# Performance work log

Measured on AMD Instinct MI355X. Metric: run time of the kernel, lower is better.

## Reference

```python
import jax, jax.numpy as jnp
import numpy as np

N_NODES = 50000
N_EDGES = 1600000
IN_DIM = 16
HID = 128
N_ITER = 3
EPS = 1e-8


def _rownorm(x):
    # x / (||x||_2 per row + 1e-8), matching torch.norm(p='fro', dim=1, keepdim=True)
    return x / (jnp.linalg.norm(x, axis=-1, keepdims=True) + EPS)


def setup_inputs() -> dict:
    key = jax.random.key(0)
    ks = jax.random.split(key, 16)
    s = 0.05  # small init scale for numerical sanity
    inp = {
        'feat': jax.random.normal(ks[0], (N_NODES, IN_DIM), dtype=jnp.float32),
        'src': jax.random.randint(ks[1], (N_EDGES,), 0, N_NODES, dtype=jnp.int32),
        'dst': jax.random.randint(ks[2], (N_EDGES,), 0, N_NODES, dtype=jnp.int32),
        'init_W0': jax.random.normal(ks[3], (IN_DIM, HID), dtype=jnp.float32) * s,
        'init_b0': jnp.zeros((HID,), dtype=jnp.float32),
        'init_W1': jax.random.normal(ks[4], (HID, HID), dtype=jnp.float32) * s,
        'init_b1': jnp.zeros((HID,), dtype=jnp.float32),
        'init_W2': jax.random.normal(ks[5], (HID, HID), dtype=jnp.float32) * s,
        'init_b2': jnp.zeros((HID,), dtype=jnp.float32),
        'node_W0': jax.random.normal(ks[6], (N_ITER, 3 * HID, HID), dtype=jnp.float32) * s,
        'node_b0': jnp.zeros((N_ITER, HID), dtype=jnp.float32),
        'node_W1': jax.random.normal(ks[7], (N_ITER, HID, HID), dtype=jnp.float32) * s,
        'node_b1': jnp.zeros((N_ITER, HID), dtype=jnp.float32),
        'node_W2': jax.random.normal(ks[8], (N_ITER, HID, HID), dtype=jnp.float32) * s,
        'node_b2': jnp.zeros((N_ITER, HID), dtype=jnp.float32),
    }
    return inp


def reference(feat, src, dst,
              init_W0, init_b0, init_W1, init_b1, init_W2, init_b2,
              node_W0, node_b0, node_W1, node_b1, node_W2, node_b2):
    n = feat.shape[0]

    # init_network: MLP (Linear+ReLU for hidden layers, linear output)
    h = jax.nn.relu(feat @ init_W0 + init_b0)
    h = jax.nn.relu(h @ init_W1 + init_b1)
    h = h @ init_W2 + init_b2  # [N, HID]

    # global representation: normalized sum over all nodes (single graph)
    gr = _rownorm(jnp.sum(h, axis=0, keepdims=True))  # [1, HID]

    # DGL update_all only updates nodes with >=1 incoming edge
    deg = jax.ops.segment_sum(jnp.ones_like(src, dtype=jnp.float32), dst,
                              num_segments=n)
    has_in = (deg > 0)[:, None]  # [N, 1]

    for i in range(node_W0.shape[0]):
        # copy_u + mailbox sum == gather src features, segment-sum by dst
        msg = jax.ops.segment_sum(h[src], dst, num_segments=n)  # [N, HID]
        inp = jnp.concatenate(
            [msg, h, jnp.broadcast_to(gr, (n, gr.shape[1]))], axis=1)  # [N, 3*HID]
        out = jax.nn.relu(inp @ node_W0[i] + node_b0[i])
        out = jax.nn.relu(out @ node_W1[i] + node_b1[i])
        out = out @ node_W2[i] + node_b2[i]
        out = _rownorm(out)
        h = jnp.where(has_in, out, h)
        gr = _rownorm(jnp.sum(h, axis=0, keepdims=True))

    return h
```

## Files before the change

kernel.cpp:

```cpp
#include <hip/hip_runtime.h>
#include <hip/hip_bf16.h>

#define HID 128
#define IN_DIM 16
#define LDST 136
#define NBSH 6
#define BPAD 16
#define SRCM 0x3ffffffu
#define CH 8192
#define NBMAX 1024
#define NDPW 4

typedef unsigned short u16;
typedef __attribute__((ext_vector_type(8))) short short8;
typedef __attribute__((ext_vector_type(4))) float f32x4;

__device__ __forceinline__ u16 f2b(float f) {
    unsigned u = __float_as_uint(f);
    return (u16)((u + 0x7FFF + ((u >> 16) & 1)) >> 16);
}


__global__ __launch_bounds__(256) void hist_k(const int* __restrict__ dst, int* __restrict__ bktcnt,
                                              int E, int nb) {
    __shared__ int hist[NBMAX];
    int tid = threadIdx.x;
    int base = blockIdx.x * CH;
    int cnt = E - base; if (cnt > CH) cnt = CH;
    for (int i = tid; i < nb; i += 256) hist[i] = 0;
    __syncthreads();
    for (int j = tid; j < cnt; j += 256) atomicAdd(&hist[dst[base + j] >> NBSH], 1);
    __syncthreads();
    for (int i = tid; i < nb; i += 256) {
        int c = hist[i];
        if (c > 0) atomicAdd(&bktcnt[i], c);
    }
}

__global__ __launch_bounds__(1024) void bscan_k(const int* __restrict__ bktcnt, int* __restrict__ bktbase,
                                                int* __restrict__ bcnt, int* __restrict__ row_ptr,
                                                int nb, int n, int E) {
    __shared__ int sbuf[1024];
    int t = threadIdx.x;
    int v = (t < nb) ? bktcnt[t] : 0;
    sbuf[t] = v;
    __syncthreads();
    for (int off = 1; off < 1024; off <<= 1) {
        int a = (t >= off) ? sbuf[t - off] : 0;
        __syncthreads();
        sbuf[t] += a;
        __syncthreads();
    }
    if (t < nb) {
        int excl = sbuf[t] - v;
        bktbase[t] = excl;
        bcnt[t * BPAD] = excl;
    }
    if (t == 0) { bktbase[nb] = E; row_ptr[n] = E; }
}

__global__ __launch_bounds__(256) void bin_k(const int* __restrict__ src, const int* __restrict__ dst,
                                             int* __restrict__ bcnt, unsigned* __restrict__ ebuf,
                                             int E, int nb) {
    __shared__ unsigned stage[CH];
    __shared__ u16 sbk[CH];
    __shared__ int hist[NBMAX];
    __shared__ int lofs[NBMAX];
    __shared__ int sbase[NBMAX];
    __shared__ int scan256[256];
    int tid = threadIdx.x;
    int base = blockIdx.x * CH;
    int cnt = E - base; if (cnt > CH) cnt = CH;

    for (int i = tid; i < nb; i += 256) hist[i] = 0;
    __syncthreads();
    for (int j = tid; j < cnt; j += 256) {
        int d = dst[base + j];
        atomicAdd(&hist[d >> NBSH], 1);
    }
    __syncthreads();
    int psum[4];
    int ts = 0;
#pragma unroll
    for (int q = 0; q < 4; q++) {
        int idx = tid * 4 + q;
        int hv = (idx < nb) ? hist[idx] : 0;
        psum[q] = ts;
        ts += hv;
    }
    scan256[tid] = ts;
    __syncthreads();
    for (int off = 1; off < 256; off <<= 1) {
        int a = (tid >= off) ? scan256[tid - off] : 0;
        __syncthreads();
        scan256[tid] += a;
        __syncthreads();
    }
    int tbase = (tid > 0) ? scan256[tid - 1] : 0;
#pragma unroll
    for (int q = 0; q < 4; q++) {
        int idx = tid * 4 + q;
        if (idx < nb) lofs[idx] = tbase + psum[q];
    }
    __syncthreads();
    for (int i = tid; i < nb; i += 256) {
        int c = hist[i];
        if (c > 0) {
            int g = atomicAdd(&bcnt[i * BPAD], c);
            sbase[i] = g - lofs[i];
        }
    }
    __syncthreads();
    for (int j = tid; j < cnt; j += 256) {
        int e = base + j;
        int d = dst[e];
        int b = d >> NBSH;
        int r = atomicAdd(&lofs[b], 1);
        stage[r] = (unsigned)src[e] | ((unsigned)(d & 63) << 26);
        sbk[r] = (u16)b;
    }
    __syncthreads();
    for (int s = tid; s < cnt; s += 256) {
        int b = sbk[s];
        ebuf[sbase[b] + s] = stage[s];
    }
}

__global__ __launch_bounds__(256) void fill2_k(const unsigned* __restrict__ ebuf, const int* __restrict__ bktbase,
                                               int* __restrict__ row_ptr, int* __restrict__ deg,
                                               int* __restrict__ srcs, int n) {
    __shared__ int hist64[64];
    __shared__ int lofs[64];
    int tid = threadIdx.x;
    int b = blockIdx.x;
    int e0 = bktbase[b], e1 = bktbase[b + 1];
    if (tid < 64) hist64[tid] = 0;
    __syncthreads();
    for (int i = e0 + tid; i < e1; i += 256) atomicAdd(&hist64[ebuf[i] >> 26], 1);
    __syncthreads();
    if (tid < 64) {
        int d = hist64[tid];
        int s = d;
#pragma unroll
        for (int off = 1; off < 64; off <<= 1) {
            int t = __shfl_up(s, off);
            if (tid >= off) s += t;
        }
        int excl = e0 + s - d;
        int gi = (b << NBSH) + tid;
        if (gi < n) { row_ptr[gi] = excl; deg[gi] = d; }
        lofs[tid] = excl;
    }
    __syncthreads();
    for (int i = e0 + tid; i < e1; i += 256) {
        unsigned p = ebuf[i];
        int d = (int)(p >> 26);
        int pos = atomicAdd(&lofs[d], 1);
        srcs[pos] = (int)(p & SRCM);
    }
}


struct WJobs {
    const float* src[16];
    int dstoff[16];
    int ks[16];
};

__global__ __launch_bounds__(256) void wprep_k(WJobs j, u16* __restrict__ Wt,
                                               int* __restrict__ bktcnt, float* __restrict__ gsums,
                                               int nb, int gz) {
    int m = blockIdx.x;
    if (m == 0) {
        for (int i = threadIdx.x; i < nb; i += 256) bktcnt[i] = 0;
    } else if (m == 1) {
        for (int i = threadIdx.x; i < gz; i += 256) gsums[i] = 0.f;
    }
    const float* s = j.src[m];
    u16* d = Wt + j.dstoff[m];
    int ks = j.ks[m];
    int K = 1 << ks;
    int tot = K * HID;
    for (int idx = threadIdx.x; idx < tot; idx += 256) {
        int nn = idx >> ks;
        int kk = idx & (K - 1);
        d[idx] = f2b(s[kk * HID + nn]);
    }
}


__device__ __forceinline__ void unpack_add(uint4 v, float* a) {
    a[0] += __uint_as_float(v.x << 16);
    a[1] += __uint_as_float(v.x & 0xffff0000u);
    a[2] += __uint_as_float(v.y << 16);
    a[3] += __uint_as_float(v.y & 0xffff0000u);
    a[4] += __uint_as_float(v.z << 16);
    a[5] += __uint_as_float(v.z & 0xffff0000u);
    a[6] += __uint_as_float(v.w << 16);
    a[7] += __uint_as_float(v.w & 0xffff0000u);
}

__global__ __launch_bounds__(256) void msg_k(const u16* __restrict__ hb, const int* __restrict__ row_ptr,
                                             const int* __restrict__ srcs, u16* __restrict__ msgb, int n,
                                             const float* __restrict__ gsumIn, const float* __restrict__ Wg,
                                             const float* __restrict__ b0, float* __restrict__ grW) {
    if (blockIdx.x == gridDim.x - 1) {
        __shared__ float sred[2];
        __shared__ float sgr[HID];
        int t = threadIdx.x;
        if (t < HID) {
            float g = gsumIn[t];
            float s = g * g;
#pragma unroll
            for (int off = 1; off < 64; off <<= 1) s += __shfl_xor(s, off);
            if ((t & 63) == 0) sred[t >> 6] = s;
        }
        __syncthreads();
        if (t < HID) {
            float inv = 1.f / (sqrtf(sred[0] + sred[1]) + 1e-8f);
            sgr[t] = gsumIn[t] * inv;
        }
        __syncthreads();
        if (t < HID) {
            float a = b0[t];
#pragma unroll 4
            for (int k = 0; k < HID; k++) a += sgr[k] * Wg[k * HID + t];
            grW[t] = a;
        }
        return;
    }
    int wave = threadIdx.x >> 6, lane = threadIdx.x & 63;
    int g = lane >> 4;
    int l16 = lane & 15;
    int d0 = (blockIdx.x * 4 + wave) * NDPW;
    if (d0 >= n) return;
    int eNext = row_ptr[d0];
#pragma unroll 1
    for (int k = 0; k < NDPW; k++) {
        int d = d0 + k;
        if (d >= n) break;
        int e = eNext;
        int e1 = row_ptr[d + 1];
        eNext = e1;
        float a[8] = {0.f, 0.f, 0.f, 0.f, 0.f, 0.f, 0.f, 0.f};
        int s0 = 0, s1 = 0, s2 = 0, s3 = 0;
        if (e + 15 < e1) {
            s0 = srcs[e + g]; s1 = srcs[e + 4 + g];
            s2 = srcs[e + 8 + g]; s3 = srcs[e + 12 + g];
        }
        while (e + 15 < e1) {
            int t0 = s0, t1 = s1, t2 = s2, t3 = s3;
            int en = e + 16;
            if (en + 15 < e1) {
                s0 = srcs[en + g]; s1 = srcs[en + 4 + g];
                s2 = srcs[en + 8 + g]; s3 = srcs[en + 12 + g];
            }
            uint4 v0 = *(const uint4*)(hb + (size_t)t0 * HID + l16 * 8);
            uint4 v1 = *(const uint4*)(hb + (size_t)t1 * HID + l16 * 8);
            uint4 v2 = *(const uint4*)(hb + (size_t)t2 * HID + l16 * 8);
            uint4 v3 = *(const uint4*)(hb + (size_t)t3 * HID + l16 * 8);
            unpack_add(v0, a);
            unpack_add(v1, a);
            unpack_add(v2, a);
            unpack_add(v3, a);
            e = en;
        }
        if (e + 7 < e1) {
            int t0 = srcs[e + g], t1 = srcs[e + 4 + g];
            uint4 v0 = *(const uint4*)(hb + (size_t)t0 * HID + l16 * 8);
            uint4 v1 = *(const uint4*)(hb + (size_t)t1 * HID + l16 * 8);
            unpack_add(v0, a);
            unpack_add(v1, a);
            e += 8;
        }
        if (e + 3 < e1) {
            int s = srcs[e + g];
            uint4 v = *(const uint4*)(hb + (size_t)s * HID + l16 * 8);
            unpack_add(v, a);
            e += 4;
        }
        if (e + g < e1) {
            int s = srcs[e + g];
            uint4 v = *(const uint4*)(hb + (size_t)s * HID + l16 * 8);
            unpack_add(v, a);
        }
#pragma unroll
        for (int i = 0; i < 8; i++) {
            a[i] += __shfl_xor(a[i], 16);
            a[i] += __shfl_xor(a[i], 32);
        }
        if (g == 0) {
            uint4 o;
            o.x = (unsigned)f2b(a[0]) | ((unsigned)f2b(a[1]) << 16);
            o.y = (unsigned)f2b(a[2]) | ((unsigned)f2b(a[3]) << 16);
            o.z = (unsigned)f2b(a[4]) | ((unsigned)f2b(a[5]) << 16);
            o.w = (unsigned)f2b(a[6]) | ((unsigned)f2b(a[7]) << 16);
            *(uint4*)(msgb + (size_t)d * HID + l16 * 8) = o;
        }
    }
}


__device__ __forceinline__ void load_tile(const u16* __restrict__ base, int tid, uint4 p[4]) {
#pragma unroll
    for (int q = 0; q < 4; q++) {
        int c = tid + q * 512;
        p[q] = *(const uint4*)(base + (size_t)(c >> 4) * HID + (c & 15) * 8);
    }
}

__device__ __forceinline__ void write_tile(const uint4 p[4], int tid, u16* s) {
#pragma unroll
    for (int q = 0; q < 4; q++) {
        int c = tid + q * 512;
        *(uint4*)(s + (c >> 4) * LDST + (c & 15) * 8) = p[q];
    }
}

__device__ __forceinline__ void stageFeat(const float* __restrict__ feat, int row0, int n, int tid, u16* sA) {
    int row = tid >> 2, coff = tid & 3;
    ushort4 o = make_ushort4(0, 0, 0, 0);
    if (row0 + row < n) {
        float4 v = *(const float4*)(feat + (size_t)(row0 + row) * IN_DIM + coff * 4);
        o = make_ushort4(f2b(v.x), f2b(v.y), f2b(v.z), f2b(v.w));
    }
    *(ushort4*)(sA + row * LDST + coff * 4) = o;
    *(ushort4*)(sA + row * LDST + 16 + coff * 4) = make_ushort4(0, 0, 0, 0);
}

__device__ __forceinline__ void stageW16(const u16* __restrict__ Wt, int tid, u16* sB) {
    if (tid < 256) {
        int row = tid >> 1, h8 = tid & 1;
        uint4 v = *(const uint4*)(Wt + row * IN_DIM + h8 * 8);
        *(uint4*)(sB + row * LDST + h8 * 8) = v;
        *(uint4*)(sB + row * LDST + 16 + h8 * 8) = make_uint4(0, 0, 0, 0);
    }
}

template <int KSTEPS>
__device__ __forceinline__ void mac(const u16* sA, const u16* sB, int wrow, int wcol,
                                    int ln15, int quad, f32x4 acc[2][4]) {
#pragma unroll
    for (int kk = 0; kk < KSTEPS; kk++) {
        short8 a[2], b[4];
#pragma unroll
        for (int mi = 0; mi < 2; mi++)
            a[mi] = *(const short8*)(sA + (wrow + mi * 16 + ln15) * LDST + kk * 32 + quad * 8);
#pragma unroll
        for (int ni = 0; ni < 4; ni++)
            b[ni] = *(const short8*)(sB + (wcol + ni * 16 + ln15) * LDST + kk * 32 + quad * 8);
#pragma unroll
        for (int mi = 0; mi < 2; mi++)
#pragma unroll
            for (int ni = 0; ni < 4; ni++)
                acc[mi][ni] = __builtin_amdgcn_mfma_f32_16x16x32_bf16(a[mi], b[ni], acc[mi][ni], 0, 0, 0);
    }
}

__device__ __forceinline__ void set_bias(f32x4 acc[2][4], const float* __restrict__ bias, int wcol, int ln15) {
#pragma unroll
    for (int ni = 0; ni < 4; ni++) {
        float bv = bias[wcol + ni * 16 + ln15];
#pragma unroll
        for (int mi = 0; mi < 2; mi++) acc[mi][ni] = (f32x4){bv, bv, bv, bv};
    }
}

__device__ __forceinline__ void acc_to_sA(const f32x4 acc[2][4], u16* sA, int wrow, int wcol,
                                          int ln15, int quad) {
#pragma unroll
    for (int mi = 0; mi < 2; mi++)
#pragma unroll
        for (int r = 0; r < 4; r++) {
            int row = wrow + mi * 16 + quad * 4 + r;
#pragma unroll
            for (int ni = 0; ni < 4; ni++)
                sA[row * LDST + wcol + ni * 16 + ln15] = f2b(fmaxf(acc[mi][ni][r], 0.f));
        }
}


__global__ __launch_bounds__(512, 4) void init_fused_k(const float* __restrict__ feat,
                                                       const u16* __restrict__ W0t, const u16* __restrict__ W1t,
                                                       const u16* __restrict__ W2t,
                                                       const float* __restrict__ b0, const float* __restrict__ b1,
                                                       const float* __restrict__ b2,
                                                       float* __restrict__ h, u16* __restrict__ hb,
                                                       float* __restrict__ gsum0, int n) {
    __shared__ u16 sA[128 * LDST];
    __shared__ u16 sB[128 * LDST];
    int tid = threadIdx.x;
    int lane = tid & 63, wave = tid >> 6;
    int ln15 = lane & 15, quad = lane >> 4;
    int wrow = (wave >> 1) * 32, wcol = (wave & 1) * 64;
    int row0 = blockIdx.x * 128;
    f32x4 acc[2][4];
    uint4 pB[4];

    stageFeat(feat, row0, n, tid, sA);
    stageW16(W0t, tid, sB);
    load_tile(W1t, tid, pB);
    set_bias(acc, b0, wcol, ln15);
    __syncthreads();
    mac<1>(sA, sB, wrow, wcol, ln15, quad, acc);
    __syncthreads();
    acc_to_sA(acc, sA, wrow, wcol, ln15, quad);
    write_tile(pB, tid, sB);
    load_tile(W2t, tid, pB);
    set_bias(acc, b1, wcol, ln15);
    __syncthreads();
    mac<4>(sA, sB, wrow, wcol, ln15, quad, acc);
    __syncthreads();
    acc_to_sA(acc, sA, wrow, wcol, ln15, quad);
    write_tile(pB, tid, sB);
    set_bias(acc, b2, wcol, ln15);
    __syncthreads();
    mac<4>(sA, sB, wrow, wcol, ln15, quad, acc);

    float csum[4] = {0.f, 0.f, 0.f, 0.f};
#pragma unroll
    for (int mi = 0; mi < 2; mi++)
#pragma unroll
        for (int r = 0; r < 4; r++) {
            int row = row0 + wrow + mi * 16 + quad * 4 + r;
            if (row < n) {
#pragma unroll
                for (int ni = 0; ni < 4; ni++) {
                    float v = acc[mi][ni][r];
                    int col = wcol + ni * 16 + ln15;
                    h[(size_t)row * HID + col] = v;
                    hb[(size_t)row * HID + col] = f2b(v);
                    csum[ni] += v;
                }
            }
        }
    __syncthreads();
    float* s_cs = (float*)sA;
    if (tid < HID) s_cs[tid] = 0.f;
    __syncthreads();
#pragma unroll
    for (int ni = 0; ni < 4; ni++) {
        float p = csum[ni];
        p += __shfl_xor(p, 16);
        p += __shfl_xor(p, 32);
        if (quad == 0) atomicAdd(&s_cs[wcol + ni * 16 + ln15], p);
    }
    __syncthreads();
    if (tid < HID) atomicAdd(&gsum0[tid], s_cs[tid]);
}


template <bool FINAL>
__global__ __launch_bounds__(512, 4) void node_fused_k(const u16* __restrict__ msgb, const u16* __restrict__ hbin,
                                                       const u16* __restrict__ W0a, const u16* __restrict__ W0b,
                                                       const u16* __restrict__ W1t, const u16* __restrict__ W2t,
                                                       const float* __restrict__ grW,
                                                       const float* __restrict__ b1, const float* __restrict__ b2,
                                                       const int* __restrict__ deg,
                                                       float* __restrict__ h, u16* __restrict__ hb,
                                                       float* __restrict__ gsumOut, int n) {
    __shared__ u16 sA[128 * LDST];
    __shared__ u16 sB[128 * LDST];
    int tid = threadIdx.x;
    int lane = tid & 63, wave = tid >> 6;
    int ln15 = lane & 15, quad = lane >> 4;
    int wrow = (wave >> 1) * 32, wcol = (wave & 1) * 64;
    int row0 = blockIdx.x * 128;
    f32x4 acc[2][4];
    uint4 pA[4], pB[4];

    load_tile(msgb + (size_t)row0 * HID, tid, pA);
    load_tile(W0a, tid, pB);
    write_tile(pA, tid, sA);
    write_tile(pB, tid, sB);
    load_tile(hbin + (size_t)row0 * HID, tid, pA);
    load_tile(W0b, tid, pB);
    set_bias(acc, grW, wcol, ln15);
    __syncthreads();
    mac<4>(sA, sB, wrow, wcol, ln15, quad, acc);
    __syncthreads();
    write_tile(pA, tid, sA);
    write_tile(pB, tid, sB);
    load_tile(W1t, tid, pB);
    __syncthreads();
    mac<4>(sA, sB, wrow, wcol, ln15, quad, acc);
    __syncthreads();
    acc_to_sA(acc, sA, wrow, wcol, ln15, quad);
    write_tile(pB, tid, sB);
    load_tile(W2t, tid, pB);
    set_bias(acc, b1, wcol, ln15);
    __syncthreads();
    mac<4>(sA, sB, wrow, wcol, ln15, quad, acc);
    __syncthreads();
    acc_to_sA(acc, sA, wrow, wcol, ln15, quad);
    write_tile(pB, tid, sB);
    set_bias(acc, b2, wcol, ln15);
    __syncthreads();
    mac<4>(sA, sB, wrow, wcol, ln15, quad, acc);

    __syncthreads();
    float* s_rs = (float*)sA;
    float* s_cs = (float*)sA + 128;
    if (tid < 128) s_rs[tid] = 0.f;
    else if (tid < 256) s_cs[tid - 128] = 0.f;
    __syncthreads();
#pragma unroll
    for (int mi = 0; mi < 2; mi++)
#pragma unroll
        for (int r = 0; r < 4; r++) {
            float p = 0.f;
#pragma unroll
            for (int ni = 0; ni < 4; ni++) { float v = acc[mi][ni][r]; p += v * v; }
            p += __shfl_xor(p, 1); p += __shfl_xor(p, 2);
            p += __shfl_xor(p, 4); p += __shfl_xor(p, 8);
            if (ln15 == 0) atomicAdd(&s_rs[wrow + mi * 16 + quad * 4 + r], p);
        }
    __syncthreads();
    float csum[4] = {0.f, 0.f, 0.f, 0.f};
#pragma unroll
    for (int mi = 0; mi < 2; mi++)
#pragma unroll
        for (int r = 0; r < 4; r++) {
            int rl = wrow + mi * 16 + quad * 4 + r;
            int row = row0 + rl;
            if (row < n) {
                bool upd = deg[row] > 0;
                float inv = 1.f / (sqrtf(s_rs[rl]) + 1e-8f);
#pragma unroll
                for (int ni = 0; ni < 4; ni++) {
                    int col = wcol + ni * 16 + ln15;
                    if (FINAL) {
                        if (upd) h[(size_t)row * HID + col] = acc[mi][ni][r] * inv;
                    } else {
                        float v;
                        if (upd) {
                            v = acc[mi][ni][r] * inv;
                            hb[(size_t)row * HID + col] = f2b(v);
                        } else {
                            v = h[(size_t)row * HID + col];
                        }
                        csum[ni] += v;
                    }
                }
            }
        }
    if (!FINAL) {
#pragma unroll
        for (int ni = 0; ni < 4; ni++) {
            float p = csum[ni];
            p += __shfl_xor(p, 16);
            p += __shfl_xor(p, 32);
            if (quad == 0) atomicAdd(&s_cs[wcol + ni * 16 + ln15], p);
        }
        __syncthreads();
        if (tid < HID) atomicAdd(&gsumOut[tid], s_cs[tid]);
    }
}


static inline char* align_up(char* p, size_t a) {
    return (char*)(((uintptr_t)p + a - 1) & ~(uintptr_t)(a - 1));
}

extern "C" void kernel_launch(void* const* d_in, const int* in_sizes, int n_in,
                              void* d_out, int out_size, void* d_ws, size_t ws_size,
                              hipStream_t stream) {
    const float* feat = (const float*)d_in[0];
    const int* src = (const int*)d_in[1];
    const int* dst = (const int*)d_in[2];
    const float* iW0 = (const float*)d_in[3];
    const float* ib0 = (const float*)d_in[4];
    const float* iW1 = (const float*)d_in[5];
    const float* ib1 = (const float*)d_in[6];
    const float* iW2 = (const float*)d_in[7];
    const float* ib2 = (const float*)d_in[8];
    const float* nW0 = (const float*)d_in[9];
    const float* nb0 = (const float*)d_in[10];
    const float* nW1 = (const float*)d_in[11];
    const float* nb1 = (const float*)d_in[12];
    const float* nW2 = (const float*)d_in[13];
    const float* nb2 = (const float*)d_in[14];

    int N = in_sizes[0] / IN_DIM;
    int E = in_sizes[1];
    int n_iter = in_sizes[10] / HID;
    int NB = (N + (1 << NBSH) - 1) >> NBSH;
    float* h = (float*)d_out;

    char* w = (char*)d_ws;
    size_t big2 = (size_t)(N + 128) * HID * sizeof(u16);
    u16* hb   = (u16*)w; w += big2;
    u16* msgb = (u16*)w; w += big2;
    float* gsums = (float*)w; w += (size_t)(n_iter + 1) * HID * sizeof(float);
    float* grW = (float*)w; w += 1024;
    u16* Wt = (u16*)w; w += (size_t)(2048 + 2 * 16384 + n_iter * 4 * 16384) * sizeof(u16);
    w = align_up(w, 16);
    int* deg = (int*)w; w += (size_t)N * 4;  w = align_up(w, 16);
    int* row_ptr = (int*)w; w += (size_t)(N + 1) * 4;  w = align_up(w, 16);
    int* bktcnt = (int*)w; w += (size_t)NB * 4;  w = align_up(w, 16);
    int* bktbase = (int*)w; w += (size_t)(NB + 1) * 4;  w = align_up(w, 64);
    int* bcnt = (int*)w; w += (size_t)NB * BPAD * 4;  w = align_up(w, 16);
    int* srcs = (int*)w; w += (size_t)E * 4;  w = align_up(w, 16);
    unsigned* ebuf = (unsigned*)w; w += (size_t)E * 4;
    (void)ws_size; (void)n_in; (void)out_size;

    const int OFF_IW0 = 0;
    const int OFF_IW1 = 2048;
    const int OFF_IW2 = 2048 + 16384;
    const int OFF_IT = 2048 + 2 * 16384;

    WJobs jobs;
    int nj = 0;
    jobs.src[nj] = iW0; jobs.dstoff[nj] = OFF_IW0; jobs.ks[nj] = 4; nj++;
    jobs.src[nj] = iW1; jobs.dstoff[nj] = OFF_IW1; jobs.ks[nj] = 7; nj++;
    jobs.src[nj] = iW2; jobs.dstoff[nj] = OFF_IW2; jobs.ks[nj] = 7; nj++;
    for (int i = 0; i < n_iter && nj + 4 <= 16; i++) {
        int base = OFF_IT + i * 4 * 16384;
        jobs.src[nj] = nW0 + (size_t)i * 3 * HID * HID;               jobs.dstoff[nj] = base;             jobs.ks[nj] = 7; nj++;
        jobs.src[nj] = nW0 + (size_t)i * 3 * HID * HID + HID * HID;   jobs.dstoff[nj] = base + 16384;     jobs.ks[nj] = 7; nj++;
        jobs.src[nj] = nW1 + (size_t)i * HID * HID;                   jobs.dstoff[nj] = base + 2 * 16384; jobs.ks[nj] = 7; nj++;
        jobs.src[nj] = nW2 + (size_t)i * HID * HID;                   jobs.dstoff[nj] = base + 3 * 16384; jobs.ks[nj] = 7; nj++;
    }

    wprep_k<<<nj, 256, 0, stream>>>(jobs, Wt, bktcnt, gsums, NB, (n_iter + 1) * HID);

    int cg = (E + CH - 1) / CH;
    hist_k<<<cg, 256, 0, stream>>>(dst, bktcnt, E, NB);
    bscan_k<<<1, 1024, 0, stream>>>(bktcnt, bktbase, bcnt, row_ptr, NB, N, E);
    bin_k<<<cg, 256, 0, stream>>>(src, dst, bcnt, ebuf, E, NB);
    fill2_k<<<NB, 256, 0, stream>>>(ebuf, bktbase, row_ptr, deg, srcs, N);

    int gb = (N + 127) / 128;
    int dpb = 4 * NDPW;
    int rb = (N + dpb - 1) / dpb;
    init_fused_k<<<gb, 512, 0, stream>>>(feat, Wt + OFF_IW0, Wt + OFF_IW1, Wt + OFF_IW2,
                                         ib0, ib1, ib2, h, hb, gsums, N);

    for (int i = 0; i < n_iter; i++) {
        const u16* Wit = Wt + OFF_IT + (size_t)i * 4 * 16384;
        const float* Wg = nW0 + (size_t)i * 3 * HID * HID + 2 * HID * HID;
        msg_k<<<rb + 1, 256, 0, stream>>>(hb, row_ptr, srcs, msgb, N,
                                          gsums + (size_t)i * HID, Wg, nb0 + (size_t)i * HID, grW);
        if (i + 1 < n_iter) {
            node_fused_k<false><<<gb, 512, 0, stream>>>(msgb, hb, Wit, Wit + 16384, Wit + 2 * 16384,
                                                        Wit + 3 * 16384, grW, nb1 + (size_t)i * HID,
                                                        nb2 + (size_t)i * HID, deg, h, hb,
                                                        gsums + (size_t)(i + 1) * HID, N);
        } else {
            node_fused_k<true><<<gb, 512, 0, stream>>>(msgb, hb, Wit, Wit + 16384, Wit + 2 * 16384,
                                                       Wit + 3 * 16384, grW, nb1 + (size_t)i * HID,
                                                       nb2 + (size_t)i * HID, deg, h, hb,
                                                       nullptr, N);
        }
    }
}
```

Before: 443.1 us.

## Fuse message aggregation and global-rep projection into node MLP kernel

Removes the separate msg_k launch. The neighbour gather-sum is now done inside the node MLP kernel, written straight into shared memory as the first MFMA operand, and each block recomputes the global-representation projection. The bf16 node features are double-buffered (ping-pong) so blocks can read the old features while writing the new ones. This avoids a global round trip for msgb and two kernel launches. In exchange, each 512-thread block with large LDS runs a serial, latency-bound gather over 128 rows, which may hide latency worse than the old fine-grained kernel. Every block also redundantly recomputes a 128x128 GEMV.

```diff
diff --git a/kernel.cpp b/kernel.cpp
--- a/kernel.cpp
+++ b/kernel.cpp
@@ -9,7 +9,6 @@
 #define SRCM 0x3ffffffu
 #define CH 8192
 #define NBMAX 1024
-#define NDPW 4
 
 typedef unsigned short u16;
 typedef __attribute__((ext_vector_type(8))) short short8;
@@ -188,7 +187,6 @@
     }
 }
 
-
 __device__ __forceinline__ void unpack_add(uint4 v, float* a) {
     a[0] += __uint_as_float(v.x << 16);
     a[1] += __uint_as_float(v.x & 0xffff0000u);
@@ -200,106 +198,6 @@
     a[7] += __uint_as_float(v.w & 0xffff0000u);
 }
 
-__global__ __launch_bounds__(256) void msg_k(const u16* __restrict__ hb, const int* __restrict__ row_ptr,
-                                             const int* __restrict__ srcs, u16* __restrict__ msgb, int n,
-                                             const float* __restrict__ gsumIn, const float* __restrict__ Wg,
-                                             const float* __restrict__ b0, float* __restrict__ grW) {
-    if (blockIdx.x == gridDim.x - 1) {
-        __shared__ float sred[2];
-        __shared__ float sgr[HID];
-        int t = threadIdx.x;
-        if (t < HID) {
-            float g = gsumIn[t];
-            float s = g * g;
-#pragma unroll
-            for (int off = 1; off < 64; off <<= 1) s += __shfl_xor(s, off);
-            if ((t & 63) == 0) sred[t >> 6] = s;
-        }
-        __syncthreads();
-        if (t < HID) {
-            float inv = 1.f / (sqrtf(sred[0] + sred[1]) + 1e-8f);
-            sgr[t] = gsumIn[t] * inv;
-        }
-        __syncthreads();
-        if (t < HID) {
-            float a = b0[t];
-#pragma unroll 4
-            for (int k = 0; k < HID; k++) a += sgr[k] * Wg[k * HID + t];
-            grW[t] = a;
-        }
-        return;
-    }
-    int wave = threadIdx.x >> 6, lane = threadIdx.x & 63;
-    int g = lane >> 4;
-    int l16 = lane & 15;
-    int d0 = (blockIdx.x * 4 + wave) * NDPW;
-    if (d0 >= n) return;
-    int eNext = row_ptr[d0];
-#pragma unroll 1
-    for (int k = 0; k < NDPW; k++) {
-        int d = d0 + k;
-        if (d >= n) break;
-        int e = eNext;
-        int e1 = row_ptr[d + 1];
-        eNext = e1;
-        float a[8] = {0.f, 0.f, 0.f, 0.f, 0.f, 0.f, 0.f, 0.f};
-        int s0 = 0, s1 = 0, s2 = 0, s3 = 0;
-        if (e + 15 < e1) {
-            s0 = srcs[e + g]; s1 = srcs[e + 4 + g];
-            s2 = srcs[e + 8 + g]; s3 = srcs[e + 12 + g];
-        }
-        while (e + 15 < e1) {
-            int t0 = s0, t1 = s1, t2 = s2, t3 = s3;
-            int en = e + 16;
-            if (en + 15 < e1) {
-                s0 = srcs[en + g]; s1 = srcs[en + 4 + g];
-                s2 = srcs[en + 8 + g]; s3 = srcs[en + 12 + g];
-            }
-            uint4 v0 = *(const uint4*)(hb + (size_t)t0 * HID + l16 * 8);
-            uint4 v1 = *(const uint4*)(hb + (size_t)t1 * HID + l16 * 8);
-            uint4 v2 = *(const uint4*)(hb + (size_t)t2 * HID + l16 * 8);
-            uint4 v3 = *(const uint4*)(hb + (size_t)t3 * HID + l16 * 8);
-            unpack_add(v0, a);
-            unpack_add(v1, a);
-            unpack_add(v2, a);
-            unpack_add(v3, a);
-            e = en;
-        }
-        if (e + 7 < e1) {
-            int t0 = srcs[e + g], t1 = srcs[e + 4 + g];
-            uint4 v0 = *(const uint4*)(hb + (size_t)t0 * HID + l16 * 8);
-            uint4 v1 = *(const uint4*)(hb + (size_t)t1 * HID + l16 * 8);
-            unpack_add(v0, a);
-            unpack_add(v1, a);
-            e += 8;
-        }
-        if (e + 3 < e1) {
-            int s = srcs[e + g];
-            uint4 v = *(const uint4*)(hb + (size_t)s * HID + l16 * 8);
-            unpack_add(v, a);
-            e += 4;
-        }
-        if (e + g < e1) {
-            int s = srcs[e + g];
-            uint4 v = *(const uint4*)(hb + (size_t)s * HID + l16 * 8);
-            unpack_add(v, a);
-        }
-#pragma unroll
-        for (int i = 0; i < 8; i++) {
-            a[i] += __shfl_xor(a[i], 16);
-            a[i] += __shfl_xor(a[i], 32);
-        }
-        if (g == 0) {
-            uint4 o;
-            o.x = (unsigned)f2b(a[0]) | ((unsigned)f2b(a[1]) << 16);
-            o.y = (unsigned)f2b(a[2]) | ((unsigned)f2b(a[3]) << 16);
-            o.z = (unsigned)f2b(a[4]) | ((unsigned)f2b(a[5]) << 16);
-            o.w = (unsigned)f2b(a[6]) | ((unsigned)f2b(a[7]) << 16);
-            *(uint4*)(msgb + (size_t)d * HID + l16 * 8) = o;
-        }
-    }
-}
-
 
 __device__ __forceinline__ void load_tile(const u16* __restrict__ base, int tid, uint4 p[4]) {
 #pragma unroll
@@ -357,7 +255,7 @@
     }
 }
 
-__device__ __forceinline__ void set_bias(f32x4 acc[2][4], const float* __restrict__ bias, int wcol, int ln15) {
+__device__ __forceinline__ void set_bias(f32x4 acc[2][4], const float* bias, int wcol, int ln15) {
 #pragma unroll
     for (int ni = 0; ni < 4; ni++) {
         float bv = bias[wcol + ni * 16 + ln15];
@@ -451,16 +349,19 @@
 
 
 template <bool FINAL>
-__global__ __launch_bounds__(512, 4) void node_fused_k(const u16* __restrict__ msgb, const u16* __restrict__ hbin,
-                                                       const u16* __restrict__ W0a, const u16* __restrict__ W0b,
-                                                       const u16* __restrict__ W1t, const u16* __restrict__ W2t,
-                                                       const float* __restrict__ grW,
-                                                       const float* __restrict__ b1, const float* __restrict__ b2,
-                                                       const int* __restrict__ deg,
-                                                       float* __restrict__ h, u16* __restrict__ hb,
-                                                       float* __restrict__ gsumOut, int n) {
+__global__ __launch_bounds__(512, 4) void node_merged_k(const u16* __restrict__ hbR, u16* __restrict__ hbW,
+                                                        const int* __restrict__ row_ptr, const int* __restrict__ srcs,
+                                                        const u16* __restrict__ W0a, const u16* __restrict__ W0b,
+                                                        const u16* __restrict__ W1t, const u16* __restrict__ W2t,
+                                                        const float* __restrict__ gsumIn, const float* __restrict__ Wg,
+                                                        const float* __restrict__ b0v, const float* __restrict__ b1,
+                                                        const float* __restrict__ b2, const int* __restrict__ deg,
+                                                        float* __restrict__ h, float* __restrict__ gsumOut, int n) {
     __shared__ u16 sA[128 * LDST];
     __shared__ u16 sB[128 * LDST];
+    __shared__ float sgp[4][HID];
+    __shared__ float sgrw[HID];
+    __shared__ float sred[2];
     int tid = threadIdx.x;
     int lane = tid & 63, wave = tid >> 6;
     int ln15 = lane & 15, quad = lane >> 4;
@@ -469,14 +370,111 @@
     f32x4 acc[2][4];
     uint4 pA[4], pB[4];
 
-    load_tile(msgb + (size_t)row0 * HID, tid, pA);
+    if (tid < HID) {
+        float g = gsumIn[tid];
+        float s = g * g;
+#pragma unroll
+        for (int off = 1; off < 64; off <<= 1) s += __shfl_xor(s, off);
+        if ((tid & 63) == 0) sred[tid >> 6] = s;
+    }
+    __syncthreads();
+    {
+        float inv = 1.f / (sqrtf(sred[0] + sred[1]) + 1e-8f);
+        int col = tid & 127, kq = tid >> 7;
+#pragma unroll 8
+        for (int k2 = 0; k2 < 32; k2++) {
+            if (k2 == 0) sgp[kq][col] = 0.f;
+        }
+        float p = 0.f;
+#pragma unroll 8
+        for (int k2 = 0; k2 < 32; k2++) {
+            int k = kq * 32 + k2;
+            p += gsumIn[k] * Wg[(size_t)k * HID + col];
+        }
+        sgp[kq][col] = p;
+        __syncthreads();
+        if (tid < HID) sgrw[tid] = b0v[tid] + inv * (sgp[0][tid] + sgp[1][tid] + sgp[2][tid] + sgp[3][tid]);
+    }
+
     load_tile(W0a, tid, pB);
-    write_tile(pA, tid, sA);
+    load_tile(hbR + (size_t)row0 * HID, tid, pA);
+
+    {
+        int gg = quad;
+        int gl = ln15;
+        int d0 = row0 + wave * 16;
+#pragma unroll 1
+        for (int k = 0; k < 16; k++) {
+            int d = d0 + k;
+            int rl = wave * 16 + k;
+            if (d >= n) {
+                if (gg == 0) *(uint4*)(sA + (size_t)rl * LDST + gl * 8) = make_uint4(0, 0, 0, 0);
+                continue;
+            }
+            int e = row_ptr[d];
+            int e1 = row_ptr[d + 1];
+            float a[8] = {0.f, 0.f, 0.f, 0.f, 0.f, 0.f, 0.f, 0.f};
+            int s0 = 0, s1 = 0, s2 = 0, s3 = 0;
+            if (e + 15 < e1) {
+                s0 = srcs[e + gg]; s1 = srcs[e + 4 + gg];
+                s2 = srcs[e + 8 + gg]; s3 = srcs[e + 12 + gg];
+            }
+            while (e + 15 < e1) {
+                int t0 = s0, t1 = s1, t2 = s2, t3 = s3;
+                int en = e + 16;
+                if (en + 15 < e1) {
+                    s0 = srcs[en + gg]; s1 = srcs[en + 4 + gg];
+                    s2 = srcs[en + 8 + gg]; s3 = srcs[en + 12 + gg];
+                }
+                uint4 v0 = *(const uint4*)(hbR + (size_t)t0 * HID + gl * 8);
+                uint4 v1 = *(const uint4*)(hbR + (size_t)t1 * HID + gl * 8);
+                uint4 v2 = *(const uint4*)(hbR + (size_t)t2 * HID + gl * 8);
+                uint4 v3 = *(const uint4*)(hbR + (size_t)t3 * HID + gl * 8);
+                unpack_add(v0, a);
+                unpack_add(v1, a);
+                unpack_add(v2, a);
+                unpack_add(v3, a);
+                e = en;
+            }
+            if (e + 7 < e1) {
+                int t0 = srcs[e + gg], t1 = srcs[e + 4 + gg];
+                uint4 v0 = *(const uint4*)(hbR + (size_t)t0 * HID + gl * 8);
+                uint4 v1 = *(const uint4*)(hbR + (size_t)t1 * HID + gl * 8);
+                unpack_add(v0, a);
+                unpack_add(v1, a);
+                e += 8;
+            }
+            if (e + 3 < e1) {
+                int s = srcs[e + gg];
+                uint4 v = *(const uint4*)(hbR + (size_t)s * HID + gl * 8);
+                unpack_add(v, a);
+                e += 4;
+            }
+            if (e + gg < e1) {
+                int s = srcs[e + gg];
+                uint4 v = *(const uint4*)(hbR + (size_t)s * HID + gl * 8);
+                unpack_add(v, a);
+            }
+#pragma unroll
+            for (int i = 0; i < 8; i++) {
+                a[i] += __shfl_xor(a[i], 16);
+                a[i] += __shfl_xor(a[i], 32);
+            }
+            if (gg == 0) {
+                uint4 o;
+                o.x = (unsigned)f2b(a[0]) | ((unsigned)f2b(a[1]) << 16);
+                o.y = (unsigned)f2b(a[2]) | ((unsigned)f2b(a[3]) << 16);
+                o.z = (unsigned)f2b(a[4]) | ((unsigned)f2b(a[5]) << 16);
+                o.w = (unsigned)f2b(a[6]) | ((unsigned)f2b(a[7]) << 16);
+                *(uint4*)(sA + (size_t)rl * LDST + gl * 8) = o;
+            }
+        }
+    }
+
     write_tile(pB, tid, sB);
-    load_tile(hbin + (size_t)row0 * HID, tid, pA);
     load_tile(W0b, tid, pB);
-    set_bias(acc, grW, wcol, ln15);
-    __syncthreads();
+    __syncthreads();
+    set_bias(acc, sgrw, wcol, ln15);
     mac<4>(sA, sB, wrow, wcol, ln15, quad, acc);
     __syncthreads();
     write_tile(pA, tid, sA);
@@ -535,10 +533,10 @@
                         float v;
                         if (upd) {
                             v = acc[mi][ni][r] * inv;
-                            hb[(size_t)row * HID + col] = f2b(v);
                         } else {
                             v = h[(size_t)row * HID + col];
                         }
+                        hbW[(size_t)row * HID + col] = f2b(v);
                         csum[ni] += v;
                     }
                 }
@@ -589,8 +587,8 @@
 
     char* w = (char*)d_ws;
     size_t big2 = (size_t)(N + 128) * HID * sizeof(u16);
-    u16* hb   = (u16*)w; w += big2;
-    u16* msgb = (u16*)w; w += big2;
+    u16* hb0  = (u16*)w; w += big2;
+    u16* hb1  = (u16*)w; w += big2;
     float* gsums = (float*)w; w += (size_t)(n_iter + 1) * HID * sizeof(float);
     float* grW = (float*)w; w += 1024;
     u16* Wt = (u16*)w; w += (size_t)(2048 + 2 * 16384 + n_iter * 4 * 16384) * sizeof(u16);
@@ -602,7 +600,7 @@
     int* bcnt = (int*)w; w += (size_t)NB * BPAD * 4;  w = align_up(w, 16);
     int* srcs = (int*)w; w += (size_t)E * 4;  w = align_up(w, 16);
     unsigned* ebuf = (unsigned*)w; w += (size_t)E * 4;
-    (void)ws_size; (void)n_in; (void)out_size;
+    (void)ws_size; (void)n_in; (void)out_size; (void)grW;
 
     const int OFF_IW0 = 0;
     const int OFF_IW1 = 2048;
@@ -631,26 +629,27 @@
     fill2_k<<<NB, 256, 0, stream>>>(ebuf, bktbase, row_ptr, deg, srcs, N);
 
     int gb = (N + 127) / 128;
-    int dpb = 4 * NDPW;
-    int rb = (N + dpb - 1) / dpb;
     init_fused_k<<<gb, 512, 0, stream>>>(feat, Wt + OFF_IW0, Wt + OFF_IW1, Wt + OFF_IW2,
-                                         ib0, ib1, ib2, h, hb, gsums, N);
-
+                                         ib0, ib1, ib2, h, hb0, gsums, N);
+
+    const u16* cur = hb0;
+    u16* nxt = hb1;
     for (int i = 0; i < n_iter; i++) {
         const u16* Wit = Wt + OFF_IT + (size_t)i * 4 * 16384;
         const float* Wg = nW0 + (size_t)i * 3 * HID * HID + 2 * HID * HID;
-        msg_k<<<rb + 1, 256, 0, stream>>>(hb, row_ptr, srcs, msgb, N,
-                                          gsums + (size_t)i * HID, Wg, nb0 + (size_t)i * HID, grW);
         if (i + 1 < n_iter) {
-            node_fused_k<false><<<gb, 512, 0, stream>>>(msgb, hb, Wit, Wit + 16384, Wit + 2 * 16384,
-                                                        Wit + 3 * 16384, grW, nb1 + (size_t)i * HID,
-                                                        nb2 + (size_t)i * HID, deg, h, hb,
-                                                        gsums + (size_t)(i + 1) * HID, N);
+            node_merged_k<false><<<gb, 512, 0, stream>>>(cur, nxt, row_ptr, srcs,
+                                                         Wit, Wit + 16384, Wit + 2 * 16384, Wit + 3 * 16384,
+                                                         gsums + (size_t)i * HID, Wg, nb0 + (size_t)i * HID,
+                                                         nb1 + (size_t)i * HID, nb2 + (size_t)i * HID, deg,
+                                                         h, gsums + (size_t)(i + 1) * HID, N);
         } else {
-            node_fused_k<true><<<gb, 512, 0, stream>>>(msgb, hb, Wit, Wit + 16384, Wit + 2 * 16384,
-                                                       Wit + 3 * 16384, grW, nb1 + (size_t)i * HID,
-                                                       nb2 + (size_t)i * HID, deg, h, hb,
-                                                       nullptr, N);
-        }
-    }
-}
+            node_merged_k<true><<<gb, 512, 0, stream>>>(cur, nxt, row_ptr, srcs,
+                                                        Wit, Wit + 16384, Wit + 2 * 16384, Wit + 3 * 16384,
+                                                        gsums + (size_t)i * HID, Wg, nb0 + (size_t)i * HID,
+                                                        nb1 + (size_t)i * HID, nb2 + (size_t)i * HID, deg,
+                                                        h, nullptr, N);
+        }
+        u16* t = (u16*)cur; cur = nxt; nxt = t;
+    }
+}
```

Measured after the change: 463.9 us. 1.05x slower.

## Pre-swizzle node MLP weights into MFMA fragment order and read from global

Applied to the files above, without the earlier changes.

Weight preparation for the per-iteration node MLP now writes the bf16 weights in the exact per-lane MFMA B-fragment order. The node kernel then loads B operands straight from global/L2 instead of staging them in shared memory. The node kernel also shrinks to 64-row tiles with 256 threads and a single shared buffer, cutting LDS use and the weight staging and barrier work per block. The cost is repeated global weight reads per block (L2-resident), plus twice as many blocks.

```diff
diff --git a/kernel.cpp b/kernel.cpp
--- a/kernel.cpp
+++ b/kernel.cpp
@@ -179,6 +179,19 @@
     const float* s = j.src[m];
     u16* d = Wt + j.dstoff[m];
     int ks = j.ks[m];
+    if (ks == 8) {
+        for (int idx = threadIdx.x; idx < 16384; idx += 256) {
+            int jj = idx & 7;
+            int lane = (idx >> 3) & 63;
+            int ni = (idx >> 9) & 3;
+            int kk = (idx >> 11) & 3;
+            int half = idx >> 13;
+            int k = kk * 32 + (lane >> 4) * 8 + jj;
+            int col = half * 64 + ni * 16 + (lane & 15);
+            d[idx] = f2b(s[k * HID + col]);
+        }
+        return;
+    }
     int K = 1 << ks;
     int tot = K * HID;
     for (int idx = threadIdx.x; idx < tot; idx += 256) {
@@ -317,6 +330,22 @@
     }
 }
 
+__device__ __forceinline__ void load_tile64(const u16* __restrict__ base, int tid, uint4 p[4]) {
+#pragma unroll
+    for (int q = 0; q < 4; q++) {
+        int c = tid + q * 256;
+        p[q] = *(const uint4*)(base + (size_t)(c >> 4) * HID + (c & 15) * 8);
+    }
+}
+
+__device__ __forceinline__ void write_tile64(const uint4 p[4], int tid, u16* s) {
+#pragma unroll
+    for (int q = 0; q < 4; q++) {
+        int c = tid + q * 256;
+        *(uint4*)(s + (c >> 4) * LDST + (c & 15) * 8) = p[q];
+    }
+}
+
 __device__ __forceinline__ void stageFeat(const float* __restrict__ feat, int row0, int n, int tid, u16* sA) {
     int row = tid >> 2, coff = tid & 3;
     ushort4 o = make_ushort4(0, 0, 0, 0);
@@ -357,7 +386,27 @@
     }
 }
 
-__device__ __forceinline__ void set_bias(f32x4 acc[2][4], const float* __restrict__ bias, int wcol, int ln15) {
+__device__ __forceinline__ void macF(const u16* sA, const u16* __restrict__ Wf, int wrow, int half,
+                                     int lane, int ln15, int quad, f32x4 acc[2][4]) {
+    const u16* wb = Wf + (size_t)half * 8192;
+#pragma unroll
+    for (int kk = 0; kk < 4; kk++) {
+        short8 a[2], b[4];
+#pragma unroll
+        for (int mi = 0; mi < 2; mi++)
+            a[mi] = *(const short8*)(sA + (wrow + mi * 16 + ln15) * LDST + kk * 32 + quad * 8);
+#pragma unroll
+        for (int ni = 0; ni < 4; ni++)
+            b[ni] = *(const short8*)(wb + (size_t)(((kk * 4 + ni) * 64) + lane) * 8);
+#pragma unroll
+        for (int mi = 0; mi < 2; mi++)
+#pragma unroll
+            for (int ni = 0; ni < 4; ni++)
+                acc[mi][ni] = __builtin_amdgcn_mfma_f32_16x16x32_bf16(a[mi], b[ni], acc[mi][ni], 0, 0, 0);
+    }
+}
+
+__device__ __forceinline__ void set_bias(f32x4 acc[2][4], const float* bias, int wcol, int ln15) {
 #pragma unroll
     for (int ni = 0; ni < 4; ni++) {
         float bv = bias[wcol + ni * 16 + ln15];
@@ -451,58 +500,52 @@
 
 
 template <bool FINAL>
-__global__ __launch_bounds__(512, 4) void node_fused_k(const u16* __restrict__ msgb, const u16* __restrict__ hbin,
-                                                       const u16* __restrict__ W0a, const u16* __restrict__ W0b,
-                                                       const u16* __restrict__ W1t, const u16* __restrict__ W2t,
+__global__ __launch_bounds__(256, 4) void node_fused_k(const u16* __restrict__ msgb, const u16* __restrict__ hbin,
+                                                       const u16* __restrict__ W0af, const u16* __restrict__ W0bf,
+                                                       const u16* __restrict__ W1f, const u16* __restrict__ W2f,
                                                        const float* __restrict__ grW,
                                                        const float* __restrict__ b1, const float* __restrict__ b2,
                                                        const int* __restrict__ deg,
                                                        float* __restrict__ h, u16* __restrict__ hb,
                                                        float* __restrict__ gsumOut, int n) {
-    __shared__ u16 sA[128 * LDST];
-    __shared__ u16 sB[128 * LDST];
+    __shared__ u16 sA[64 * LDST];
     int tid = threadIdx.x;
     int lane = tid & 63, wave = tid >> 6;
     int ln15 = lane & 15, quad = lane >> 4;
-    int wrow = (wave >> 1) * 32, wcol = (wave & 1) * 64;
-    int row0 = blockIdx.x * 128;
+    int wrow = (wave >> 1) * 32, half = wave & 1, wcol = half * 64;
+    int row0 = blockIdx.x * 64;
     f32x4 acc[2][4];
-    uint4 pA[4], pB[4];
-
-    load_tile(msgb + (size_t)row0 * HID, tid, pA);
-    load_tile(W0a, tid, pB);
-    write_tile(pA, tid, sA);
-    write_tile(pB, tid, sB);
-    load_tile(hbin + (size_t)row0 * HID, tid, pA);
-    load_tile(W0b, tid, pB);
+
+    {
+        uint4 tM[4];
+        load_tile64(msgb + (size_t)row0 * HID, tid, tM);
+        write_tile64(tM, tid, sA);
+    }
+    uint4 tH[4];
+    load_tile64(hbin + (size_t)row0 * HID, tid, tH);
     set_bias(acc, grW, wcol, ln15);
     __syncthreads();
-    mac<4>(sA, sB, wrow, wcol, ln15, quad, acc);
-    __syncthreads();
-    write_tile(pA, tid, sA);
-    write_tile(pB, tid, sB);
-    load_tile(W1t, tid, pB);
-    __syncthreads();
-    mac<4>(sA, sB, wrow, wcol, ln15, quad, acc);
+    macF(sA, W0af, wrow, half, lane, ln15, quad, acc);
+    __syncthreads();
+    write_tile64(tH, tid, sA);
+    __syncthreads();
+    macF(sA, W0bf, wrow, half, lane, ln15, quad, acc);
     __syncthreads();
     acc_to_sA(acc, sA, wrow, wcol, ln15, quad);
-    write_tile(pB, tid, sB);
-    load_tile(W2t, tid, pB);
     set_bias(acc, b1, wcol, ln15);
     __syncthreads();
-    mac<4>(sA, sB, wrow, wcol, ln15, quad, acc);
+    macF(sA, W1f, wrow, half, lane, ln15, quad, acc);
     __syncthreads();
     acc_to_sA(acc, sA, wrow, wcol, ln15, quad);
-    write_tile(pB, tid, sB);
     set_bias(acc, b2, wcol, ln15);
     __syncthreads();
-    mac<4>(sA, sB, wrow, wcol, ln15, quad, acc);
+    macF(sA, W2f, wrow, half, lane, ln15, quad, acc);
 
     __syncthreads();
     float* s_rs = (float*)sA;
-    float* s_cs = (float*)sA + 128;
-    if (tid < 128) s_rs[tid] = 0.f;
-    else if (tid < 256) s_cs[tid - 128] = 0.f;
+    float* s_cs = (float*)sA + 64;
+    if (tid < 64) s_rs[tid] = 0.f;
+    else if (tid < 192) s_cs[tid - 64] = 0.f;
     __syncthreads();
 #pragma unroll
     for (int mi = 0; mi < 2; mi++)
@@ -616,10 +659,10 @@
     jobs.src[nj] = iW2; jobs.dstoff[nj] = OFF_IW2; jobs.ks[nj] = 7; nj++;
     for (int i = 0; i < n_iter && nj + 4 <= 16; i++) {
         int base = OFF_IT + i * 4 * 16384;
-        jobs.src[nj] = nW0 + (size_t)i * 3 * HID * HID;               jobs.dstoff[nj] = base;             jobs.ks[nj] = 7; nj++;
-        jobs.src[nj] = nW0 + (size_t)i * 3 * HID * HID + HID * HID;   jobs.dstoff[nj] = base + 16384;     jobs.ks[nj] = 7; nj++;
-        jobs.src[nj] = nW1 + (size_t)i * HID * HID;                   jobs.dstoff[nj] = base + 2 * 16384; jobs.ks[nj] = 7; nj++;
-        jobs.src[nj] = nW2 + (size_t)i * HID * HID;                   jobs.dstoff[nj] = base + 3 * 16384; jobs.ks[nj] = 7; nj++;
+        jobs.src[nj] = nW0 + (size_t)i * 3 * HID * HID;               jobs.dstoff[nj] = base;             jobs.ks[nj] = 8; nj++;
+        jobs.src[nj] = nW0 + (size_t)i * 3 * HID * HID + HID * HID;   jobs.dstoff[nj] = base + 16384;     jobs.ks[nj] = 8; nj++;
+        jobs.src[nj] = nW1 + (size_t)i * HID * HID;                   jobs.dstoff[nj] = base + 2 * 16384; jobs.ks[nj] = 8; nj++;
+        jobs.src[nj] = nW2 + (size_t)i * HID * HID;                   jobs.dstoff[nj] = base + 3 * 16384; jobs.ks[nj] = 8; nj++;
     }
 
     wprep_k<<<nj, 256, 0, stream>>>(jobs, Wt, bktcnt, gsums, NB, (n_iter + 1) * HID);
@@ -631,6 +674,7 @@
     fill2_k<<<NB, 256, 0, stream>>>(ebuf, bktbase, row_ptr, deg, srcs, N);
 
     int gb = (N + 127) / 128;
+    int gb2 = (N + 63) / 64;
     int dpb = 4 * NDPW;
     int rb = (N + dpb - 1) / dpb;
     init_fused_k<<<gb, 512, 0, stream>>>(feat, Wt + OFF_IW0, Wt + OFF_IW1, Wt + OFF_IW2,
@@ -642,15 +686,15 @@
         msg_k<<<rb + 1, 256, 0, stream>>>(hb, row_ptr, srcs, msgb, N,
                                           gsums + (size_t)i * HID, Wg, nb0 + (size_t)i * HID, grW);
         if (i + 1 < n_iter) {
-            node_fused_k<false><<<gb, 512, 0, stream>>>(msgb, hb, Wit, Wit + 16384, Wit + 2 * 16384,
+            node_fused_k<false><<<gb2, 256, 0, stream>>>(msgb, hb, Wit, Wit + 16384, Wit + 2 * 16384,
+                                                         Wit + 3 * 16384, grW, nb1 + (size_t)i * HID,
+                                                         nb2 + (size_t)i * HID, deg, h, hb,
+                                                         gsums + (size_t)(i + 1) * HID, N);
+        } else {
+            node_fused_k<true><<<gb2, 256, 0, stream>>>(msgb, hb, Wit, Wit + 16384, Wit + 2 * 16384,
                                                         Wit + 3 * 16384, grW, nb1 + (size_t)i * HID,
                                                         nb2 + (size_t)i * HID, deg, h, hb,
-                                                        gsums + (size_t)(i + 1) * HID, N);
-        } else {
-            node_fused_k<true><<<gb, 512, 0, stream>>>(msgb, hb, Wit, Wit + 16384, Wit + 2 * 16384,
-                                                       Wit + 3 * 16384, grW, nb1 + (size_t)i * HID,
-                                                       nb2 + (size_t)i * HID, deg, h, hb,
-                                                       nullptr, N);
-        }
-    }
-}
+                                                        nullptr, N);
+        }
+    }
+}
```

New measurement: 440.8 us. Within noise of the previous version (-0.5%).
